# Optimization experiments

Hardware: AMD Instinct MI355X
Metric: run time of the kernel (lower is better)

Reference implementation:

```python
import jax, jax.numpy as jnp
import numpy as np

N = 10000   # nodes
E = 320000  # edges
D = 256     # in_dim == hidden_dim
H = 4       # heads
DK = 64     # head dim
BN_EPS = 1e-5


def _relu6(x):
    return jnp.clip(x, 0.0, 6.0)


def setup_inputs() -> dict:
    key = jax.random.key(0)
    ks = jax.random.split(key, 16)
    rn = lambda k, shape, s=0.05: jax.random.normal(k, shape, dtype=jnp.float32) * s
    return {
        "v": jax.random.normal(ks[0], (N, D), dtype=jnp.float32),
        "WQ": rn(ks[1], (D, D)), "bQ": jnp.zeros((D,), jnp.float32),
        "WK": rn(ks[2], (D, D)), "bK": jnp.zeros((D,), jnp.float32),
        "WV": rn(ks[3], (D, D)), "bV": jnp.zeros((D,), jnp.float32),
        "Wo": rn(ks[4], (D, D)), "bo": jnp.zeros((D,), jnp.float32),
        "W1": rn(ks[5], (D, 64)), "b1": jnp.zeros((64,), jnp.float32),
        "W2": rn(ks[6], (64, D)), "b2": jnp.zeros((D,), jnp.float32),
        "gamma": jnp.ones((D,), jnp.float32),
        "beta": jnp.zeros((D,), jnp.float32),
        "src": jax.random.randint(ks[7], (E,), 0, N),
        "dst": jax.random.randint(ks[8], (E,), 0, N),
    }


def reference(v, WQ, bQ, WK, bK, WV, bV, Wo, bo, W1, b1, W2, b2, gamma, beta, src, dst):
    ones_e = jnp.ones((E,), jnp.float32)
    # center weighting: softmax over (in_degree + out_degree)
    deg = (jax.ops.segment_sum(ones_e, src, num_segments=N)
           + jax.ops.segment_sum(ones_e, dst, num_segments=N))
    center = jax.nn.softmax(deg)                      # [N]
    mV = v * center[:, None]                          # [N, D]

    q = (mV @ WQ + bQ).reshape(N, H, DK)
    k = (mV @ WK + bK).reshape(N, H, DK)
    vv = (mV @ WV + bV).reshape(N, H, DK)

    # edge score: dot(k[src], q[dst]) per head, clamped scaled exp
    score = jnp.einsum('ehd,ehd->eh', k[src], q[dst])  # [E, H]
    s = jnp.exp(jnp.clip(score / np.sqrt(DK), -5.0, 5.0))

    wv = jax.ops.segment_sum(vv[src] * s[:, :, None], dst, num_segments=N)  # [N,H,DK]
    z = jax.ops.segment_sum(s, dst, num_segments=N)                         # [N,H]

    o = (wv / z[:, :, None]).reshape(N, D) @ Wo + bo   # output projection

    # BatchNorm1d (training-mode batch stats, biased var) + ReLU6
    mean = jnp.mean(o, axis=0)
    var = jnp.mean((o - mean) ** 2, axis=0)
    x = _relu6(gamma * (o - mean) / jnp.sqrt(var + BN_EPS) + beta)

    # SE block: Linear -> ReLU6 -> Linear -> HardSwish
    se = _relu6(x @ W1 + b1) @ W2 + b2
    se = se * _relu6(se + 3.0) / 6.0

    return se * x + v
```

## Files before the change

kernel.cpp:

```cpp
#include <hip/hip_runtime.h>
#include <math.h>

#define N_NODES 10000
#define N_EDGES 320000
#define DIM 256
#define ND ((size_t)N_NODES * DIM)

typedef float f32x4 __attribute__((ext_vector_type(4)));
typedef short s16x8 __attribute__((ext_vector_type(8)));
typedef short s16x4 __attribute__((ext_vector_type(4)));

__device__ __forceinline__ float relu6f(float x) { return fminf(fmaxf(x, 0.f), 6.f); }

__device__ __forceinline__ short f2bf(float x) {
  unsigned u = __builtin_bit_cast(unsigned, x);
  unsigned r = (u + 0x7fffu + ((u >> 16) & 1u)) >> 16;
  return (short)r;
}
__device__ __forceinline__ float bf2f(short b) {
  unsigned u = ((unsigned)(unsigned short)b) << 16;
  return __builtin_bit_cast(float, u);
}
__device__ __forceinline__ float bflo(unsigned u) {
  return __builtin_bit_cast(float, u << 16);
}
__device__ __forceinline__ float bfhi(unsigned u) {
  return __builtin_bit_cast(float, u & 0xffff0000u);
}

__global__ __launch_bounds__(256) void k_prologue(
    const float* __restrict__ WQ, const float* __restrict__ WK,
    const float* __restrict__ WV, const float* __restrict__ Wo,
    const float* __restrict__ W1, const float* __restrict__ W2,
    short* __restrict__ Wt_hi, short* __restrict__ Wt_lo,
    short* __restrict__ W1h, short* __restrict__ W1l,
    short* __restrict__ W2h, short* __restrict__ W2l,
    const int* __restrict__ src, const int* __restrict__ dst,
    int* __restrict__ outc, int* __restrict__ inc) {
  __shared__ float tile[64][65];
  int bid = blockIdx.x, t = threadIdx.x;
  if (bid < 72) {
    const float* W;
    short *hi, *lo;
    int K, N, tk, tn;
    if (bid < 64) {
      int mat = bid >> 4, tl = bid & 15;
      W = (mat == 0) ? WQ : (mat == 1) ? WK : (mat == 2) ? WV : Wo;
      hi = Wt_hi + (size_t)mat * 65536;
      lo = Wt_lo + (size_t)mat * 65536;
      K = 256; N = 256;
      tk = (tl >> 2) * 64; tn = (tl & 3) * 64;
    } else if (bid < 68) {
      W = W1; hi = W1h; lo = W1l;
      K = 256; N = 64;
      tk = (bid - 64) * 64; tn = 0;
    } else {
      W = W2; hi = W2h; lo = W2l;
      K = 64; N = 256;
      tk = 0; tn = (bid - 68) * 64;
    }
    int r = t >> 4, c4 = (t & 15) * 4;
#pragma unroll
    for (int p = 0; p < 4; p++) {
      float4 v4 = *(const float4*)(W + (size_t)(tk + p * 16 + r) * N + tn + c4);
      tile[p * 16 + r][c4 + 0] = v4.x;
      tile[p * 16 + r][c4 + 1] = v4.y;
      tile[p * 16 + r][c4 + 2] = v4.z;
      tile[p * 16 + r][c4 + 3] = v4.w;
    }
    __syncthreads();
    int nl = t >> 2, q = t & 3;
    s16x8 h0, h1, l0, l1;
#pragma unroll
    for (int j = 0; j < 8; j++) {
      float x = tile[q * 16 + j][nl];
      short hb = f2bf(x);
      h0[j] = hb; l0[j] = f2bf(x - bf2f(hb));
    }
#pragma unroll
    for (int j = 0; j < 8; j++) {
      float x = tile[q * 16 + 8 + j][nl];
      short hb = f2bf(x);
      h1[j] = hb; l1[j] = f2bf(x - bf2f(hb));
    }
    size_t base = (size_t)(tn + nl) * K + tk + q * 16;
    *(s16x8*)(hi + base) = h0;
    *(s16x8*)(hi + base + 8) = h1;
    *(s16x8*)(lo + base) = l0;
    *(s16x8*)(lo + base + 8) = l1;
  } else {
    int e = (bid - 72) * 256 + t;
    if (e < N_EDGES) {
      atomicAdd(&outc[src[e]], 1);
      atomicAdd(&inc[dst[e]], 1);
    }
  }
}

__global__ void k_scan(const int* __restrict__ inc, const int* __restrict__ outc,
                       int* __restrict__ rowptr, int* __restrict__ nextp,
                       float* __restrict__ logzf) {
  __shared__ int wsum[16];
  __shared__ double dsum[16];
  __shared__ int carry_s;
  int tid = threadIdx.x, lane = tid & 63, wid = tid >> 6;

  double e = 0.0;
  for (int i = tid; i < N_NODES; i += 1024) e += exp((double)(inc[i] + outc[i]));
#pragma unroll
  for (int off = 1; off < 64; off <<= 1) e += __shfl_xor(e, off);
  if (lane == 0) dsum[wid] = e;
  __syncthreads();
  if (tid == 0) {
    double Z = 0.0;
#pragma unroll
    for (int i = 0; i < 16; i++) Z += dsum[i];
    logzf[0] = (float)log(Z);
    carry_s = 0;
  }
  __syncthreads();

  for (int base = 0; base < N_NODES; base += 1024) {
    int i = base + tid;
    int v = (i < N_NODES) ? inc[i] : 0;
    int x = v;
#pragma unroll
    for (int off = 1; off < 64; off <<= 1) {
      int t = __shfl_up(x, off);
      if (lane >= off) x += t;
    }
    if (lane == 63) wsum[wid] = x;
    __syncthreads();
    if (wid == 0 && lane < 16) {
      int wv = wsum[lane];
#pragma unroll
      for (int off = 1; off < 16; off <<= 1) {
        int t = __shfl_up(wv, off);
        if (lane >= off) wv += t;
      }
      wsum[lane] = wv;
    }
    __syncthreads();
    int carry = carry_s;
    int wadd = (wid > 0) ? wsum[wid - 1] : 0;
    int excl = carry + wadd + x - v;
    if (i < N_NODES) {
      rowptr[i] = excl;
      nextp[i] = excl;
    }
    __syncthreads();
    if (tid == 1023) carry_s = excl + v;
    __syncthreads();
  }
  if (tid == 0) rowptr[N_NODES] = carry_s;
}

__global__ __launch_bounds__(256) void k_fillsplit(
    const int* __restrict__ src, const int* __restrict__ dst,
    int* __restrict__ nextp, int* __restrict__ csr_src,
    const float* __restrict__ v, const int* __restrict__ inc,
    const int* __restrict__ outc, const float* __restrict__ logzf,
    short* __restrict__ Ahg, short* __restrict__ Alg) {
  int bid = blockIdx.x, t = threadIdx.x;
  int e = bid * 256 + t;
  if (e < N_EDGES) {
    int pos = atomicAdd(&nextp[dst[e]], 1);
    csr_src[pos] = src[e];
  }
  size_t idx = ((size_t)bid * 256 + t) * 4;
  int row = (int)(idx >> 8);
  float c = __expf((float)(inc[row] + outc[row]) - logzf[0]);
  float4 x = *(const float4*)(v + idx);
  float xs[4] = {x.x * c, x.y * c, x.z * c, x.w * c};
  s16x4 h, l;
#pragma unroll
  for (int j = 0; j < 4; j++) {
    short hb = f2bf(xs[j]);
    h[j] = hb;
    l[j] = f2bf(xs[j] - bf2f(hb));
  }
  *(s16x4*)(Ahg + idx) = h;
  *(s16x4*)(Alg + idx) = l;
}

template <int KVMODE>
__global__ __launch_bounds__(256) void k_gemm_mfma(
    const short* __restrict__ Ahg, const short* __restrict__ Alg,
    const short* __restrict__ Whi, const short* __restrict__ Wlo,
    const float* __restrict__ b0, const float* __restrict__ b1,
    const float* __restrict__ b2, float* __restrict__ Qout,
    unsigned short* __restrict__ KVout, float* __restrict__ Cbase,
    float* __restrict__ bnsum, float* __restrict__ bnsq, int M) {
  const float* bias = (blockIdx.z == 0) ? b0 : (blockIdx.z == 1) ? b1 : b2;
  const short* whi = Whi + (size_t)blockIdx.z * 65536;
  const short* wlo = Wlo + (size_t)blockIdx.z * 65536;

  __shared__ __align__(16) short Ah[64][40];
  __shared__ __align__(16) short Al[64][40];
  __shared__ __align__(16) short Bh[128][40];
  __shared__ __align__(16) short Bl[128][40];

  int tid = threadIdx.x;
  int lane = tid & 63, wid = tid >> 6;
  int wm = wid >> 1, wn = wid & 1;
  int m0 = blockIdx.x * 64;
  int n0g = blockIdx.y * 128;

  f32x4 acc[2][4];
#pragma unroll
  for (int i = 0; i < 2; i++)
#pragma unroll
    for (int j = 0; j < 4; j++) acc[i][j] = (f32x4){0.f, 0.f, 0.f, 0.f};

  int sa_row = tid >> 2, sa_seg = tid & 3;
  int sb_row = tid >> 1, sb_seg = tid & 1;
  const s16x8 zero8 = {0, 0, 0, 0, 0, 0, 0, 0};

  for (int k0 = 0; k0 < 256; k0 += 32) {
    __syncthreads();
    {
      int m = m0 + sa_row;
      s16x8 h = zero8, l = zero8;
      if (m < M) {
        size_t ga = (size_t)m * 256 + k0 + sa_seg * 8;
        h = *(const s16x8*)(Ahg + ga);
        l = *(const s16x8*)(Alg + ga);
      }
      *(s16x8*)&Ah[sa_row][sa_seg * 8] = h;
      *(s16x8*)&Al[sa_row][sa_seg * 8] = l;
    }
    {
      size_t gb = (size_t)(n0g + sb_row) * 256 + k0 + sb_seg * 16;
      *(s16x8*)&Bh[sb_row][sb_seg * 16] = *(const s16x8*)(whi + gb);
      *(s16x8*)&Bh[sb_row][sb_seg * 16 + 8] = *(const s16x8*)(whi + gb + 8);
      *(s16x8*)&Bl[sb_row][sb_seg * 16] = *(const s16x8*)(wlo + gb);
      *(s16x8*)&Bl[sb_row][sb_seg * 16 + 8] = *(const s16x8*)(wlo + gb + 8);
    }
    __syncthreads();
    int arow0 = wm * 32 + (lane & 15);
    int kc = (lane >> 4) * 8;
    s16x8 ah[2], al[2], bh[4], bl[4];
#pragma unroll
    for (int mf = 0; mf < 2; mf++) {
      ah[mf] = *(const s16x8*)&Ah[arow0 + mf * 16][kc];
      al[mf] = *(const s16x8*)&Al[arow0 + mf * 16][kc];
    }
    int brow0 = wn * 64 + (lane & 15);
#pragma unroll
    for (int nf = 0; nf < 4; nf++) {
      bh[nf] = *(const s16x8*)&Bh[brow0 + nf * 16][kc];
      bl[nf] = *(const s16x8*)&Bl[brow0 + nf * 16][kc];
    }
#pragma unroll
    for (int mf = 0; mf < 2; mf++)
#pragma unroll
      for (int nf = 0; nf < 4; nf++) {
        acc[mf][nf] = __builtin_amdgcn_mfma_f32_16x16x32_bf16(ah[mf], bh[nf], acc[mf][nf], 0, 0, 0);
        acc[mf][nf] = __builtin_amdgcn_mfma_f32_16x16x32_bf16(al[mf], bh[nf], acc[mf][nf], 0, 0, 0);
        acc[mf][nf] = __builtin_amdgcn_mfma_f32_16x16x32_bf16(ah[mf], bl[nf], acc[mf][nf], 0, 0, 0);
      }
  }

  int colq = lane & 15, rowq = (lane >> 4) * 4;
  if (KVMODE == 1) {
    bool isq = (blockIdx.z == 0);
    int kvoff = (blockIdx.z == 1) ? 0 : 256;
#pragma unroll
    for (int mf = 0; mf < 2; mf++) {
#pragma unroll
      for (int nf = 0; nf < 4; nf++) {
        int n = wn * 64 + nf * 16 + colq;
        float bv = bias[n0g + n];
#pragma unroll
        for (int j = 0; j < 4; j++) {
          int m = m0 + wm * 32 + mf * 16 + rowq + j;
          if (m >= M) continue;
          float val = acc[mf][nf][j] + bv;
          if (isq) Qout[(size_t)m * 256 + n0g + n] = val;
          else KVout[(size_t)m * 512 + kvoff + n0g + n] = (unsigned short)f2bf(val);
        }
      }
    }
  } else {
    float cs[4], cq[4];
#pragma unroll
    for (int nf = 0; nf < 4; nf++) { cs[nf] = 0.f; cq[nf] = 0.f; }
#pragma unroll
    for (int nf = 0; nf < 4; nf++) {
      int n = wn * 64 + nf * 16 + colq;
      float bv = bias[n0g + n];
#pragma unroll
      for (int mf = 0; mf < 2; mf++) {
#pragma unroll
        for (int j = 0; j < 4; j++) {
          int m = m0 + wm * 32 + mf * 16 + rowq + j;
          if (m >= M) continue;
          float val = acc[mf][nf][j] + bv;
          Cbase[(size_t)m * 256 + n0g + n] = val;
          cs[nf] += val;
          cq[nf] = fmaf(val, val, cq[nf]);
        }
      }
    }
#pragma unroll
    for (int nf = 0; nf < 4; nf++) {
      float s = cs[nf], qq = cq[nf];
      s += __shfl_xor(s, 16); s += __shfl_xor(s, 32);
      qq += __shfl_xor(qq, 16); qq += __shfl_xor(qq, 32);
      if (lane < 16) {
        int n = n0g + wn * 64 + nf * 16 + lane;
        atomicAdd(&bnsum[n], s);
        atomicAdd(&bnsq[n], qq);
      }
    }
  }
}

__global__ __launch_bounds__(256) void k_edgeagg(
    const int* __restrict__ rowptr, const int* __restrict__ csr_src,
    const float* __restrict__ q, const unsigned short* __restrict__ kv,
    short* __restrict__ att_h, short* __restrict__ att_l) {
  int lane = threadIdx.x & 63, wid = threadIdx.x >> 6;
  int n = blockIdx.x * 4 + wid;
  int beg = rowptr[n], end = rowptr[n + 1];
  float4 qv = *(const float4*)(q + (size_t)n * 256 + lane * 4);
  const unsigned short* kvl = kv + lane * 4;
  float a0 = 0.f, a1 = 0.f, a2 = 0.f, a3 = 0.f, z = 0.f;

#define EDGE_BODY(SRC)                                                        \
  {                                                                           \
    const unsigned short* rp = kvl + (size_t)(SRC) * 512;                     \
    uint2 ku = *(const uint2*)rp;                                             \
    uint2 vu = *(const uint2*)(rp + 256);                                     \
    float p = bflo(ku.x) * qv.x + bfhi(ku.x) * qv.y +                         \
              bflo(ku.y) * qv.z + bfhi(ku.y) * qv.w;                          \
    p += __shfl_xor(p, 1);                                                    \
    p += __shfl_xor(p, 2);                                                    \
    p += __shfl_xor(p, 4);                                                    \
    p += __shfl_xor(p, 8);                                                    \
    float e0 = __expf(fminf(fmaxf(p * 0.125f, -5.f), 5.f));                   \
    a0 = fmaf(e0, bflo(vu.x), a0);                                            \
    a1 = fmaf(e0, bfhi(vu.x), a1);                                            \
    a2 = fmaf(e0, bflo(vu.y), a2);                                            \
    a3 = fmaf(e0, bfhi(vu.y), a3);                                            \
    z += e0;                                                                  \
  }

  for (int base = beg; base < end; base += 64) {
    int idx = base + lane;
    int eid = (idx < end) ? csr_src[idx] : 0;
    int bs = min(64, end - base);
    int j = 0;
    for (; j + 4 <= bs; j += 4) {
      int s0 = __builtin_amdgcn_readlane(eid, j);
      int s1 = __builtin_amdgcn_readlane(eid, j + 1);
      int s2 = __builtin_amdgcn_readlane(eid, j + 2);
      int s3 = __builtin_amdgcn_readlane(eid, j + 3);
      EDGE_BODY(s0); EDGE_BODY(s1); EDGE_BODY(s2); EDGE_BODY(s3);
    }
    for (; j < bs; j++) {
      int s0 = __builtin_amdgcn_readlane(eid, j);
      EDGE_BODY(s0);
    }
  }
#undef EDGE_BODY

  float invz = 1.f / z;
  float rs[4] = {a0 * invz, a1 * invz, a2 * invz, a3 * invz};
  s16x4 h, l;
#pragma unroll
  for (int j = 0; j < 4; j++) {
    short hb = f2bf(rs[j]);
    h[j] = hb;
    l[j] = f2bf(rs[j] - bf2f(hb));
  }
  size_t base_o = (size_t)n * 256 + lane * 4;
  *(s16x4*)(att_h + base_o) = h;
  *(s16x4*)(att_l + base_o) = l;
}

__global__ __launch_bounds__(256) void k_se2(
    const float* __restrict__ o,
    const float* __restrict__ bnsum, const float* __restrict__ bnsq,
    const float* __restrict__ gamma, const float* __restrict__ beta,
    const short* __restrict__ W1h, const short* __restrict__ W1l,
    const float* __restrict__ b1,
    const short* __restrict__ W2h, const short* __restrict__ W2l,
    const float* __restrict__ b2,
    const float* __restrict__ vin, float* __restrict__ out) {
  __shared__ __align__(16) short xh[64][264];
  __shared__ __align__(16) short xl[64][264];
  __shared__ __align__(16) short hh[64][72];
  __shared__ __align__(16) short hl[64][72];
  __shared__ float vt[64][256];
  __shared__ float scale_s[256], shift_s[256];

  int t = threadIdx.x;
  int lane = t & 63, w = t >> 6;
  int m0 = blockIdx.x * 64;

  {
    float mean = bnsum[t] * (1.f / N_NODES);
    float var = bnsq[t] * (1.f / N_NODES) - mean * mean;
    float istd = rsqrtf(var + 1e-5f);
    float sc = gamma[t] * istd;
    scale_s[t] = sc;
    shift_s[t] = beta[t] - mean * sc;
  }
  __syncthreads();

  {
    int r = t >> 2;
    int cb = (t & 3) * 4;
    int gr = m0 + r;
    bool rok = gr < N_NODES;
#pragma unroll
    for (int p = 0; p < 16; p++) {
      int c = cb + p * 16;
      float4 ov = make_float4(0.f, 0.f, 0.f, 0.f), vv = ov;
      if (rok) {
        ov = *(const float4*)(o + (size_t)gr * 256 + c);
        vv = *(const float4*)(vin + (size_t)gr * 256 + c);
      }
      float xs[4];
      xs[0] = relu6f(fmaf(ov.x, scale_s[c + 0], shift_s[c + 0]));
      xs[1] = relu6f(fmaf(ov.y, scale_s[c + 1], shift_s[c + 1]));
      xs[2] = relu6f(fmaf(ov.z, scale_s[c + 2], shift_s[c + 2]));
      xs[3] = relu6f(fmaf(ov.w, scale_s[c + 3], shift_s[c + 3]));
#pragma unroll
      for (int j = 0; j < 4; j++) {
        short hb = f2bf(xs[j]);
        xh[r][c + j] = hb;
        xl[r][c + j] = f2bf(xs[j] - bf2f(hb));
      }
      *(float4*)&vt[r][c] = vv;
    }
  }
  __syncthreads();

  int fr = lane & 15, fq = lane >> 4;
  int kc = fq * 8;
  int arow = w * 16 + fr;

  f32x4 acc1[4];
#pragma unroll
  for (int nf = 0; nf < 4; nf++) acc1[nf] = (f32x4){0.f, 0.f, 0.f, 0.f};
#pragma unroll
  for (int ks = 0; ks < 8; ks++) {
    s16x8 ah = *(const s16x8*)&xh[arow][ks * 32 + kc];
    s16x8 al = *(const s16x8*)&xl[arow][ks * 32 + kc];
#pragma unroll
    for (int nf = 0; nf < 4; nf++) {
      size_t bo_ = (size_t)(nf * 16 + fr) * 256 + ks * 32 + kc;
      s16x8 bh = *(const s16x8*)(W1h + bo_);
      s16x8 bl = *(const s16x8*)(W1l + bo_);
      acc1[nf] = __builtin_amdgcn_mfma_f32_16x16x32_bf16(ah, bh, acc1[nf], 0, 0, 0);
      acc1[nf] = __builtin_amdgcn_mfma_f32_16x16x32_bf16(al, bh, acc1[nf], 0, 0, 0);
      acc1[nf] = __builtin_amdgcn_mfma_f32_16x16x32_bf16(ah, bl, acc1[nf], 0, 0, 0);
    }
  }
#pragma unroll
  for (int nf = 0; nf < 4; nf++) {
    int n = nf * 16 + fr;
    float bv = b1[n];
#pragma unroll
    for (int j = 0; j < 4; j++) {
      int row = w * 16 + fq * 4 + j;
      float hv = relu6f(acc1[nf][j] + bv);
      short hb = f2bf(hv);
      hh[row][n] = hb;
      hl[row][n] = f2bf(hv - bf2f(hb));
    }
  }
  __syncthreads();

  f32x4 acc2[16];
#pragma unroll
  for (int nf = 0; nf < 16; nf++) acc2[nf] = (f32x4){0.f, 0.f, 0.f, 0.f};
#pragma unroll
  for (int ks = 0; ks < 2; ks++) {
    s16x8 ah = *(const s16x8*)&hh[arow][ks * 32 + kc];
    s16x8 al = *(const s16x8*)&hl[arow][ks * 32 + kc];
#pragma unroll
    for (int nf = 0; nf < 16; nf++) {
      size_t bo_ = (size_t)(nf * 16 + fr) * 64 + ks * 32 + kc;
      s16x8 bh = *(const s16x8*)(W2h + bo_);
      s16x8 bl = *(const s16x8*)(W2l + bo_);
      acc2[nf] = __builtin_amdgcn_mfma_f32_16x16x32_bf16(ah, bh, acc2[nf], 0, 0, 0);
      acc2[nf] = __builtin_amdgcn_mfma_f32_16x16x32_bf16(al, bh, acc2[nf], 0, 0, 0);
      acc2[nf] = __builtin_amdgcn_mfma_f32_16x16x32_bf16(ah, bl, acc2[nf], 0, 0, 0);
    }
  }
#pragma unroll
  for (int nf = 0; nf < 16; nf++) {
    int col = nf * 16 + fr;
    float bv = b2[col];
#pragma unroll
    for (int j = 0; j < 4; j++) {
      int row = w * 16 + fq * 4 + j;
      int grow = m0 + row;
      if (grow < N_NODES) {
        float se = acc2[nf][j] + bv;
        float hs = se * relu6f(se + 3.f) * (1.f / 6.f);
        float xr = bf2f(xh[row][col]) + bf2f(xl[row][col]);
        out[(size_t)grow * 256 + col] = fmaf(hs, xr, vt[row][col]);
      }
    }
  }
}

extern "C" void kernel_launch(void* const* d_in, const int* in_sizes, int n_in,
                              void* d_out, int out_size, void* d_ws, size_t ws_size,
                              hipStream_t stream) {
  const float* v     = (const float*)d_in[0];
  const float* WQ    = (const float*)d_in[1];
  const float* bQ    = (const float*)d_in[2];
  const float* WK    = (const float*)d_in[3];
  const float* bK    = (const float*)d_in[4];
  const float* WV    = (const float*)d_in[5];
  const float* bV    = (const float*)d_in[6];
  const float* Wo    = (const float*)d_in[7];
  const float* bo    = (const float*)d_in[8];
  const float* W1    = (const float*)d_in[9];
  const float* b1    = (const float*)d_in[10];
  const float* W2    = (const float*)d_in[11];
  const float* b2    = (const float*)d_in[12];
  const float* gamma = (const float*)d_in[13];
  const float* beta  = (const float*)d_in[14];
  const int* srcI    = (const int*)d_in[15];
  const int* dstI    = (const int*)d_in[16];
  float* out = (float*)d_out;

  char* w = (char*)d_ws;
  size_t off = 0;
  auto take = [&](size_t bytes) {
    size_t o = off;
    off += (bytes + 255) & ~(size_t)255;
    return o;
  };
  int* inc      = (int*)(w + take(N_NODES * 4));
  int* outc     = (int*)(w + take(N_NODES * 4));
  float* bnsum  = (float*)(w + take(256 * 4));
  float* bnsq   = (float*)(w + take(256 * 4));
  size_t zero_span = off;
  float* logzf  = (float*)(w + take(4));
  float* q      = (float*)(w + take(ND * 4));
  unsigned short* kvb = (unsigned short*)(w + take((size_t)N_NODES * 512 * 2));
  short* Ahg    = (short*)(w + take(ND * 2));
  short* Alg    = (short*)(w + take(ND * 2));
  short* att_h  = (short*)(w + take(ND * 2));
  short* att_l  = (short*)(w + take(ND * 2));
  int* rowptr   = (int*)(w + take((N_NODES + 1) * 4));
  int* nextp    = (int*)(w + take(N_NODES * 4));
  int* csr_src  = (int*)(w + take((size_t)N_EDGES * 4));
  short* Wt_hi  = (short*)(w + take((size_t)4 * 65536 * 2));
  short* Wt_lo  = (short*)(w + take((size_t)4 * 65536 * 2));
  short* W1h    = (short*)(w + take((size_t)16384 * 2));
  short* W1l    = (short*)(w + take((size_t)16384 * 2));
  short* W2h    = (short*)(w + take((size_t)16384 * 2));
  short* W2l    = (short*)(w + take((size_t)16384 * 2));

  float* o = (float*)kvb;

  hipMemsetAsync(w, 0, zero_span, stream);

  k_prologue<<<dim3(1322), dim3(256), 0, stream>>>(
      WQ, WK, WV, Wo, W1, W2, Wt_hi, Wt_lo, W1h, W1l, W2h, W2l,
      srcI, dstI, outc, inc);

  k_scan<<<dim3(1), dim3(1024), 0, stream>>>(inc, outc, rowptr, nextp, logzf);

  k_fillsplit<<<dim3(2500), dim3(256), 0, stream>>>(
      srcI, dstI, nextp, csr_src, v, inc, outc, logzf, Ahg, Alg);

  k_gemm_mfma<1><<<dim3(157, 2, 3), dim3(256), 0, stream>>>(
      Ahg, Alg, Wt_hi, Wt_lo, bQ, bK, bV, q, kvb, nullptr, nullptr, nullptr, N_NODES);

  k_edgeagg<<<dim3(N_NODES / 4), dim3(256), 0, stream>>>(rowptr, csr_src, q, kvb, att_h, att_l);

  k_gemm_mfma<0><<<dim3(157, 2, 1), dim3(256), 0, stream>>>(
      att_h, att_l, Wt_hi + (size_t)3 * 65536, Wt_lo + (size_t)3 * 65536,
      bo, bo, bo, nullptr, nullptr, o, bnsum, bnsq, N_NODES);

  k_se2<<<dim3((N_NODES + 63) / 64), dim3(256), 0, stream>>>(
      o, bnsum, bnsq, gamma, beta, W1h, W1l, b1, W2h, W2l, b2, v, out);
}
```

Baseline: 284.1 us.

## Split edge aggregation into per-head launches with four edges per wavefront

Edge aggregation now runs as four launches, one per head. Each wavefront handles one node and one head, and its four 16-lane groups process four edges at once, with a cross-group shuffle reduction at the end. The aim is a smaller K/V working set per launch (only one head's 64-column slice is gathered) for better cache locality, plus more edge-level parallelism per wave. In exchange it issues four times the launches, re-reads the CSR indices and rowptr four times, and gathers narrow 8-byte pieces from scattered rows.

Measured after the change: 315.7 us. 1.11x slower.

```diff
diff --git a/kernel.cpp b/kernel.cpp
--- a/kernel.cpp
+++ b/kernel.cpp
@@ -316,67 +316,59 @@
   }
 }
 
-__global__ __launch_bounds__(256) void k_edgeagg(
+__global__ __launch_bounds__(256) void k_edgeagg_h(
     const int* __restrict__ rowptr, const int* __restrict__ csr_src,
     const float* __restrict__ q, const unsigned short* __restrict__ kv,
-    short* __restrict__ att_h, short* __restrict__ att_l) {
+    short* __restrict__ att_h, short* __restrict__ att_l, int head) {
   int lane = threadIdx.x & 63, wid = threadIdx.x >> 6;
   int n = blockIdx.x * 4 + wid;
   int beg = rowptr[n], end = rowptr[n + 1];
-  float4 qv = *(const float4*)(q + (size_t)n * 256 + lane * 4);
-  const unsigned short* kvl = kv + lane * 4;
+  int eg = lane >> 4, dl = lane & 15;
+  int hoff = head * 64 + dl * 4;
+  float4 qv = *(const float4*)(q + (size_t)n * 256 + hoff);
   float a0 = 0.f, a1 = 0.f, a2 = 0.f, a3 = 0.f, z = 0.f;
 
-#define EDGE_BODY(SRC)                                                        \
-  {                                                                           \
-    const unsigned short* rp = kvl + (size_t)(SRC) * 512;                     \
-    uint2 ku = *(const uint2*)rp;                                             \
-    uint2 vu = *(const uint2*)(rp + 256);                                     \
-    float p = bflo(ku.x) * qv.x + bfhi(ku.x) * qv.y +                         \
-              bflo(ku.y) * qv.z + bfhi(ku.y) * qv.w;                          \
-    p += __shfl_xor(p, 1);                                                    \
-    p += __shfl_xor(p, 2);                                                    \
-    p += __shfl_xor(p, 4);                                                    \
-    p += __shfl_xor(p, 8);                                                    \
-    float e0 = __expf(fminf(fmaxf(p * 0.125f, -5.f), 5.f));                   \
-    a0 = fmaf(e0, bflo(vu.x), a0);                                            \
-    a1 = fmaf(e0, bfhi(vu.x), a1);                                            \
-    a2 = fmaf(e0, bflo(vu.y), a2);                                            \
-    a3 = fmaf(e0, bfhi(vu.y), a3);                                            \
-    z += e0;                                                                  \
-  }
-
-  for (int base = beg; base < end; base += 64) {
-    int idx = base + lane;
-    int eid = (idx < end) ? csr_src[idx] : 0;
-    int bs = min(64, end - base);
-    int j = 0;
-    for (; j + 4 <= bs; j += 4) {
-      int s0 = __builtin_amdgcn_readlane(eid, j);
-      int s1 = __builtin_amdgcn_readlane(eid, j + 1);
-      int s2 = __builtin_amdgcn_readlane(eid, j + 2);
-      int s3 = __builtin_amdgcn_readlane(eid, j + 3);
-      EDGE_BODY(s0); EDGE_BODY(s1); EDGE_BODY(s2); EDGE_BODY(s3);
-    }
-    for (; j < bs; j++) {
-      int s0 = __builtin_amdgcn_readlane(eid, j);
-      EDGE_BODY(s0);
-    }
-  }
-#undef EDGE_BODY
-
-  float invz = 1.f / z;
-  float rs[4] = {a0 * invz, a1 * invz, a2 * invz, a3 * invz};
-  s16x4 h, l;
-#pragma unroll
-  for (int j = 0; j < 4; j++) {
-    short hb = f2bf(rs[j]);
-    h[j] = hb;
-    l[j] = f2bf(rs[j] - bf2f(hb));
-  }
-  size_t base_o = (size_t)n * 256 + lane * 4;
-  *(s16x4*)(att_h + base_o) = h;
-  *(s16x4*)(att_l + base_o) = l;
+  for (int i = beg; i < end; i += 4) {
+    int idx = i + eg;
+    bool ok = idx < end;
+    int s = ok ? csr_src[idx] : 0;
+    const unsigned short* rp = kv + (size_t)s * 512 + hoff;
+    uint2 ku = *(const uint2*)rp;
+    uint2 vu = *(const uint2*)(rp + 256);
+    float p = bflo(ku.x) * qv.x + bfhi(ku.x) * qv.y +
+              bflo(ku.y) * qv.z + bfhi(ku.y) * qv.w;
+    p += __shfl_xor(p, 1);
+    p += __shfl_xor(p, 2);
+    p += __shfl_xor(p, 4);
+    p += __shfl_xor(p, 8);
+    float e0 = ok ? __expf(fminf(fmaxf(p * 0.125f, -5.f), 5.f)) : 0.f;
+    a0 = fmaf(e0, bflo(vu.x), a0);
+    a1 = fmaf(e0, bfhi(vu.x), a1);
+    a2 = fmaf(e0, bflo(vu.y), a2);
+    a3 = fmaf(e0, bfhi(vu.y), a3);
+    z += e0;
+  }
+
+  a0 += __shfl_xor(a0, 16); a0 += __shfl_xor(a0, 32);
+  a1 += __shfl_xor(a1, 16); a1 += __shfl_xor(a1, 32);
+  a2 += __shfl_xor(a2, 16); a2 += __shfl_xor(a2, 32);
+  a3 += __shfl_xor(a3, 16); a3 += __shfl_xor(a3, 32);
+  z  += __shfl_xor(z, 16);  z  += __shfl_xor(z, 32);
+
+  if (eg == 0) {
+    float invz = 1.f / z;
+    float rs[4] = {a0 * invz, a1 * invz, a2 * invz, a3 * invz};
+    s16x4 h, l;
+#pragma unroll
+    for (int j = 0; j < 4; j++) {
+      short hb = f2bf(rs[j]);
+      h[j] = hb;
+      l[j] = f2bf(rs[j] - bf2f(hb));
+    }
+    size_t base_o = (size_t)n * 256 + hoff;
+    *(s16x4*)(att_h + base_o) = h;
+    *(s16x4*)(att_l + base_o) = l;
+  }
 }
 
 __global__ __launch_bounds__(256) void k_se2(
@@ -576,7 +568,9 @@
   k_gemm_mfma<1><<<dim3(157, 2, 3), dim3(256), 0, stream>>>(
       Ahg, Alg, Wt_hi, Wt_lo, bQ, bK, bV, q, kvb, nullptr, nullptr, nullptr, N_NODES);
 
-  k_edgeagg<<<dim3(N_NODES / 4), dim3(256), 0, stream>>>(rowptr, csr_src, q, kvb, att_h, att_l);
+  for (int h = 0; h < 4; h++)
+    k_edgeagg_h<<<dim3(N_NODES / 4), dim3(256), 0, stream>>>(
+        rowptr, csr_src, q, kvb, att_h, att_l, h);
 
   k_gemm_mfma<0><<<dim3(157, 2, 1), dim3(256), 0, stream>>>(
       att_h, att_l, Wt_hi + (size_t)3 * 65536, Wt_lo + (size_t)3 * 65536,
```
